# Kernel optimization log

Measured on AMD Instinct MI355X. Metric: run time of the kernel, lower is better.

Reference implementation:

```python
import jax, jax.numpy as jnp
import numpy as np

ALPHA = 1.5
N_ITER = 50
N_ROWS, N_CLASSES = 4096, 32000


def tsallis_bisect(X, alpha=ALPHA, n_iter=N_ITER):
    """Entmax/Tsallis simplex projection via 50-step bisection (matches
    the standard entmax-bisect forward used by sisl/EvSoftmax)."""
    d = X.shape[-1]
    exp = 1.0 / (alpha - 1.0)          # = 2.0 for alpha = 1.5
    Xs = X * (alpha - 1.0)
    max_val = jnp.max(Xs, axis=-1, keepdims=True)            # [N,1]
    tau_lo = max_val - 1.0
    tau_hi = max_val - (1.0 / d) ** (alpha - 1.0)
    f_lo = jnp.sum(jnp.clip(Xs - tau_lo, 0.0) ** exp, axis=-1, keepdims=True) - 1.0
    dm0 = tau_hi - tau_lo

    def body(carry, _):
        tau_lo, dm, _tau_m = carry
        dm = dm * 0.5
        tau_m = tau_lo + dm                                   # [N,1]
        p_m = jnp.clip(Xs - tau_m, 0.0) ** exp                # [N,d]
        f_m = jnp.sum(p_m, axis=-1, keepdims=True) - 1.0
        mask = (f_m * f_lo) >= 0
        tau_lo = jnp.where(mask, tau_m, tau_lo)
        return (tau_lo, dm, tau_m), None

    (_, _, tau_m), _ = jax.lax.scan(body, (tau_lo, dm0, tau_lo), None, length=n_iter)
    return jnp.clip(Xs - tau_m, 0.0) ** exp                   # final p_m


def setup_inputs() -> dict:
    key = jax.random.key(0)
    X = jax.random.normal(key, (N_ROWS, N_CLASSES), dtype=jnp.float32)
    return {"X": X}


def reference(X):
    p_star = tsallis_bisect(X, ALPHA, N_ITER)
    p_star = p_star / jnp.sum(p_star, axis=1, keepdims=True)
    # safe log: value identical to log(p_star) (log(0) = -inf), but with a
    # well-defined (zero) subgradient at exactly-sparse entries.
    return jnp.where(p_star > 0, jnp.log(jnp.where(p_star > 0, p_star, 1.0)), -jnp.inf)
```

## Files before the change

kernel.cpp:

```cpp
#include <hip/hip_runtime.h>
#include <math.h>


#define NCOLS    32000
#define TPBA     512
#define NFULL    15
#define TAILBASE 30720
#define TAILTHR  320
#define NWAVE    8
#define SEGB     320
#define CAPR     (SEGB * NWAVE)
#define NSLOT    (CAPR / 64)
#define MSEG     512
#define SENT16   ((unsigned short)0xC2C0)
#define CSF      0.0055901699437494742f

__device__ __forceinline__ float wred_max(float x) {
#pragma unroll
  for (int o = 1; o < 64; o <<= 1) x = fmaxf(x, __shfl_xor(x, o, 64));
  return x;
}
__device__ __forceinline__ float wred_addf(float x) {
#pragma unroll
  for (int o = 1; o < 64; o <<= 1) x += __shfl_xor(x, o, 64);
  return x;
}
__device__ __forceinline__ int lane_prefix(unsigned long long m) {
  return __builtin_amdgcn_mbcnt_hi((unsigned)(m >> 32),
         __builtin_amdgcn_mbcnt_lo((unsigned)m, 0));
}
__device__ __forceinline__ unsigned short to_bf16_safe(float x) {
  unsigned int u = __float_as_uint(x);
  u += 0x7FFFu + ((u >> 16) & 1u);
  unsigned short h = (unsigned short)(u >> 16);
  if ((h & 0x7F80u) == 0x7F80u) h = SENT16;
  return h;
}

__global__ __launch_bounds__(TPBA, 4)
void tsa_stream(const float* __restrict__ X, unsigned short* __restrict__ Out,
                float* __restrict__ tauv, int* __restrict__ cnt,
                float* __restrict__ vals, unsigned short* __restrict__ idxs) {
  __shared__ float s_redf[NWAVE];
  __shared__ int   s_ovf;
  const int t    = threadIdx.x;
  const int lane = t & 63;
  const int wid  = t >> 6;
  const size_t row = blockIdx.x;
  const float* __restrict__ xr      = X + row * (size_t)NCOLS;
  unsigned short* __restrict__ orow = Out + row * (size_t)NCOLS;

  float4 v[16];
#pragma unroll
  for (int j = 0; j < NFULL; ++j)
    v[j] = *reinterpret_cast<const float4*>(xr + j * 2048 + t * 4);
  if (t < TAILTHR)
    v[15] = *reinterpret_cast<const float4*>(xr + TAILBASE + t * 4);
  else
    v[15] = make_float4(-1e30f, -1e30f, -1e30f, -1e30f);
  if (t == 0) s_ovf = 0;

  float m = -1e30f;
#pragma unroll
  for (int j = 0; j < 16; ++j)
    m = fmaxf(m, fmaxf(fmaxf(v[j].x, v[j].y), fmaxf(v[j].z, v[j].w)));
  m = wred_max(m);
  if (lane == 0) s_redf[wid] = m;
  __syncthreads();
  float mm = s_redf[0];
#pragma unroll
  for (int w = 1; w < NWAVE; ++w) mm = fmaxf(mm, s_redf[w]);
  const float max_val = 0.5f * mm;
  const float tl0 = max_val - 1.0f;
  if (t == 0) tauv[row] = max_val;

  {
    int base = 0;
    float* __restrict__ vb = vals + row * (size_t)CAPR + wid * SEGB;
    unsigned short* __restrict__ ib = idxs + row * (size_t)CAPR + wid * SEGB;
#pragma unroll
    for (int j = 0; j < 16; ++j) {
      const int gidx = (j < NFULL) ? (j * 2048 + t * 4) : (TAILBASE + t * 4);
      const float xs[4] = {v[j].x * 0.5f, v[j].y * 0.5f,
                           v[j].z * 0.5f, v[j].w * 0.5f};
#pragma unroll
      for (int c = 0; c < 4; ++c) {
        const bool b = xs[c] > tl0;
        const unsigned long long mk = __ballot(b);
        const int tot = __popcll(mk);
        if (base + tot <= SEGB) {
          if (b) {
            const int pos = base + lane_prefix(mk);
            vb[pos] = xs[c];
            ib[pos] = (unsigned short)(gidx + c);
          }
        } else if (lane == 0) {
          s_ovf = 1;
        }
        base += tot;
      }
    }
    if (base <= SEGB && lane == 0) cnt[row * NWAVE + wid] = base;
  }
  __syncthreads();

  if (s_ovf) {
    if (t == 0) cnt[row * NWAVE] = -1;
    const float th = max_val - CSF;
    auto bsum = [&](float tau) -> float {
      float q = 0.f;
#pragma unroll
      for (int j = 0; j < 16; ++j) {
        float r;
        r = fmaxf(v[j].x * 0.5f - tau, 0.f); q = fmaf(r, r, q);
        r = fmaxf(v[j].y * 0.5f - tau, 0.f); q = fmaf(r, r, q);
        r = fmaxf(v[j].z * 0.5f - tau, 0.f); q = fmaf(r, r, q);
        r = fmaxf(v[j].w * 0.5f - tau, 0.f); q = fmaf(r, r, q);
      }
      q = wred_addf(q);
      if (lane == 0) s_redf[wid] = q;
      __syncthreads();
      float tt = s_redf[0];
#pragma unroll
      for (int w = 1; w < NWAVE; ++w) tt += s_redf[w];
      __syncthreads();
      return tt;
    };
    float tau_lo = tl0, dmv = th - tl0, tau_m = tl0;
    const float f_lo = bsum(tau_lo) - 1.0f;
#pragma unroll 1
    for (int it = 0; it < 50; ++it) {
      dmv *= 0.5f;
      const float tm = tau_lo + dmv;
      if (tm == tau_lo) { tau_m = tau_lo; break; }
      tau_m = tm;
      const float fm = bsum(tm) - 1.0f;
      if (fm * f_lo >= 0.0f) tau_lo = tm;
    }
    const float sf = bsum(tau_m);
#pragma unroll
    for (int j = 0; j < 16; ++j) {
      const bool act = (j < NFULL) || (t < TAILTHR);
      if (act) {
        const int gidx = (j < NFULL) ? (j * 2048 + t * 4) : (TAILBASE + t * 4);
        unsigned short h[4];
        float rc, pn;
        rc = fmaxf(v[j].x * 0.5f - tau_m, 0.f); pn = (rc * rc) / sf; h[0] = (pn > 0.f) ? to_bf16_safe(logf(pn)) : SENT16;
        rc = fmaxf(v[j].y * 0.5f - tau_m, 0.f); pn = (rc * rc) / sf; h[1] = (pn > 0.f) ? to_bf16_safe(logf(pn)) : SENT16;
        rc = fmaxf(v[j].z * 0.5f - tau_m, 0.f); pn = (rc * rc) / sf; h[2] = (pn > 0.f) ? to_bf16_safe(logf(pn)) : SENT16;
        rc = fmaxf(v[j].w * 0.5f - tau_m, 0.f); pn = (rc * rc) / sf; h[3] = (pn > 0.f) ? to_bf16_safe(logf(pn)) : SENT16;
        *reinterpret_cast<uint2*>(orow + gidx) =
            make_uint2((unsigned)h[0] | ((unsigned)h[1] << 16),
                       (unsigned)h[2] | ((unsigned)h[3] << 16));
      }
    }
  }
}

__global__ __launch_bounds__(512, 4)
void tsa_bisect(unsigned short* __restrict__ Out,
                const float* __restrict__ tauv, const int* __restrict__ cnt,
                const float* __restrict__ vals,
                const unsigned short* __restrict__ idxs, int nrows) {
  const int t    = threadIdx.x;
  const int lane = t & 63;
  const int wid  = t >> 6;
  const int row  = blockIdx.x * NWAVE + wid;
  if (row >= nrows) return;

  int c8 = (lane < NWAVE) ? cnt[row * NWAVE + lane] : 0;
  const int c0 = __shfl(c8, 0, 64);
  if (c0 < 0) return;

  unsigned short* __restrict__ orow = Out + (size_t)row * NCOLS;

  {
    const unsigned int sp = 0xC2C0C2C0u;
    const uint4 fillv = make_uint4(sp, sp, sp, sp);
    uint4* o4 = reinterpret_cast<uint4*>(orow);
#pragma unroll 1
    for (int r = 0; r < 63; ++r) {
      const int p = lane + r * 64;
      if (p < NCOLS / 8) o4[p] = fillv;
    }
  }

  const float* __restrict__ vb = vals + (size_t)row * CAPR;
  float cv[NSLOT];
#pragma unroll
  for (int r = 0; r < NSLOT; ++r) cv[r] = vb[lane + r * 64];
#pragma unroll
  for (int r = 0; r < NSLOT; ++r) {
    const int cs = __shfl(c8, r / 5, 64);
    if ((r % 5) * 64 + lane >= cs) cv[r] = -1e30f;
  }

  const float max_val = tauv[row];
  const float tl0 = max_val - 1.0f;
  const float th  = max_val - CSF;

  auto fsum = [&](float tau) -> float {
    float q0 = 0.f, q1 = 0.f, q2 = 0.f, q3 = 0.f;
#pragma unroll
    for (int r = 0; r < NSLOT; r += 4) {
      float a;
      a = fmaxf(cv[r + 0] - tau, 0.f); q0 = fmaf(a, a, q0);
      a = fmaxf(cv[r + 1] - tau, 0.f); q1 = fmaf(a, a, q1);
      a = fmaxf(cv[r + 2] - tau, 0.f); q2 = fmaf(a, a, q2);
      a = fmaxf(cv[r + 3] - tau, 0.f); q3 = fmaf(a, a, q3);
    }
    return wred_addf((q0 + q1) + (q2 + q3));
  };

  float tau_lo = tl0, dmv = th - tl0, tau_m = tl0;
  const float f_lo = fsum(tau_lo) - 1.0f;
#pragma unroll 1
  for (int it = 0; it < 50; ++it) {
    dmv *= 0.5f;
    const float tm = tau_lo + dmv;
    if (tm == tau_lo) { tau_m = tau_lo; break; }
    tau_m = tm;
    const float fm = fsum(tm) - 1.0f;
    if (fm * f_lo >= 0.0f) tau_lo = tm;
  }
  const float sf = fsum(tau_m);

  asm volatile("s_waitcnt vmcnt(0)" ::: "memory");

  const unsigned short* __restrict__ ib = idxs + (size_t)row * CAPR;
#pragma unroll 1
  for (int r = 0; r < NSLOT; ++r) {
    const float rc = fmaxf(cv[r] - tau_m, 0.f);
    const float pn = (rc * rc) / sf;
    if (pn > 0.f) orow[ib[lane + r * 64]] = to_bf16_safe(logf(pn));
  }
}

__global__ __launch_bounds__(TPBA, 8)
void tsa_mono(const float* __restrict__ X, unsigned short* __restrict__ Out) {
  __shared__ float          s_redf[NWAVE];
  __shared__ int            s_segk[NWAVE];
  __shared__ int            s_ovf;
  __shared__ float          s_tau, s_sf;
  __shared__ float          s_cand[MSEG * NWAVE];
  __shared__ unsigned short s_cidx[MSEG * NWAVE];

  const int t = threadIdx.x, lane = t & 63, wid = t >> 6;
  const size_t row = blockIdx.x;
  const float* __restrict__ xr      = X + row * (size_t)NCOLS;
  unsigned short* __restrict__ orow = Out + row * (size_t)NCOLS;

  float m = -1e30f;
#pragma unroll 5
  for (int j = 0; j < NFULL; ++j) {
    float4 a = *reinterpret_cast<const float4*>(xr + j * 2048 + t * 4);
    m = fmaxf(m, fmaxf(fmaxf(a.x, a.y), fmaxf(a.z, a.w)));
  }
  if (t < TAILTHR) {
    float4 a = *reinterpret_cast<const float4*>(xr + TAILBASE + t * 4);
    m = fmaxf(m, fmaxf(fmaxf(a.x, a.y), fmaxf(a.z, a.w)));
  }
  m = wred_max(m);
  if (lane == 0) s_redf[wid] = m;
  if (t == 0) s_ovf = 0;
  __syncthreads();
  float mm = s_redf[0];
#pragma unroll
  for (int w = 1; w < NWAVE; ++w) mm = fmaxf(mm, s_redf[w]);
  const float max_val = 0.5f * mm;
  const float tau_lo0 = max_val - 1.0f;
  const float tau_hi  = max_val - CSF;

  {
    int base = 0;
    const int seg0 = wid * MSEG;
    const unsigned long long SFILL = 0xC2C0C2C0C2C0C2C0ull;
#pragma unroll 2
    for (int j = 0; j <= NFULL; ++j) {
      const bool act = (j < NFULL) || (t < TAILTHR);
      const int gidx = (j < NFULL) ? (j * 2048 + t * 4) : (TAILBASE + t * 4);
      float x0 = -1e30f, x1 = -1e30f, x2 = -1e30f, x3 = -1e30f;
      if (act) {
        float4 a = *reinterpret_cast<const float4*>(xr + gidx);
        x0 = a.x * 0.5f; x1 = a.y * 0.5f; x2 = a.z * 0.5f; x3 = a.w * 0.5f;
        __builtin_nontemporal_store(
            SFILL, reinterpret_cast<unsigned long long*>(orow + gidx));
      }
      int c = (x0 > tau_lo0) + (x1 > tau_lo0) + (x2 > tau_lo0) + (x3 > tau_lo0);
      int pre = c;
#pragma unroll
      for (int o = 1; o < 64; o <<= 1) {
        int y = __shfl_up(pre, o, 64);
        if (lane >= o) pre += y;
      }
      const int tot = __shfl(pre, 63, 64);
      if (base + tot <= MSEG) {
        int pos = seg0 + base + (pre - c);
        if (x0 > tau_lo0) { s_cand[pos] = x0; s_cidx[pos] = (unsigned short)(gidx + 0); ++pos; }
        if (x1 > tau_lo0) { s_cand[pos] = x1; s_cidx[pos] = (unsigned short)(gidx + 1); ++pos; }
        if (x2 > tau_lo0) { s_cand[pos] = x2; s_cidx[pos] = (unsigned short)(gidx + 2); ++pos; }
        if (x3 > tau_lo0) { s_cand[pos] = x3; s_cidx[pos] = (unsigned short)(gidx + 3); ++pos; }
      } else if (lane == 0) {
        s_ovf = 1;
      }
      base += tot;
    }
    if (base <= MSEG) {
      const int kp = (base + 63) & ~63;
      for (int i = base + lane; i < kp; i += 64) s_cand[seg0 + i] = -1e30f;
    }
    if (lane == 0) s_segk[wid] = base;
  }
  __syncthreads();

  if (s_ovf == 0) {
    if (wid == 0) {
      int kp[NWAVE];
#pragma unroll
      for (int s = 0; s < NWAVE; ++s) kp[s] = (s_segk[s] + 63) & ~63;
      auto fsum = [&](float tau) -> float {
        float q = 0.f;
#pragma unroll 1
        for (int s = 0; s < NWAVE; ++s) {
          const float* cs = s_cand + s * MSEG;
          const int kps = kp[s];
          for (int i = lane; i < kps; i += 64) {
            const float r = fmaxf(cs[i] - tau, 0.f);
            q = fmaf(r, r, q);
          }
        }
        return wred_addf(q);
      };
      float tau_lo = tau_lo0, dmv = tau_hi - tau_lo0, tau_m = tau_lo0;
      const float f_lo = fsum(tau_lo) - 1.0f;
#pragma unroll 1
      for (int it = 0; it < 50; ++it) {
        dmv *= 0.5f;
        const float tm = tau_lo + dmv;
        if (tm == tau_lo) { tau_m = tau_lo; break; }
        tau_m = tm;
        const float fm = fsum(tm) - 1.0f;
        if (fm * f_lo >= 0.0f) tau_lo = tm;
      }
      const float sf = fsum(tau_m);
      if (lane == 0) { s_tau = tau_m; s_sf = sf; }
    }
    __syncthreads();
    const float tau_m = s_tau, sf = s_sf;
#pragma unroll 1
    for (int s = 0; s < NWAVE; ++s) {
      const int ks = s_segk[s];
      for (int i = t; i < ks; i += TPBA) {
        const float rc = fmaxf(s_cand[s * MSEG + i] - tau_m, 0.f);
        const float pn = (rc * rc) / sf;
        if (pn > 0.f) orow[s_cidx[s * MSEG + i]] = to_bf16_safe(logf(pn));
      }
    }
  } else {
    auto bsum = [&](float tau) -> float {
      float q = 0.f;
#pragma unroll 4
      for (int j = 0; j <= NFULL; ++j) {
        const bool act = (j < NFULL) || (t < TAILTHR);
        const int gidx = (j < NFULL) ? (j * 2048 + t * 4) : (TAILBASE + t * 4);
        if (act) {
          float4 a = *reinterpret_cast<const float4*>(xr + gidx);
          float r;
          r = fmaxf(a.x * 0.5f - tau, 0.f); q = fmaf(r, r, q);
          r = fmaxf(a.y * 0.5f - tau, 0.f); q = fmaf(r, r, q);
          r = fmaxf(a.z * 0.5f - tau, 0.f); q = fmaf(r, r, q);
          r = fmaxf(a.w * 0.5f - tau, 0.f); q = fmaf(r, r, q);
        }
      }
      q = wred_addf(q);
      if (lane == 0) s_redf[wid] = q;
      __syncthreads();
      float tot = s_redf[0];
#pragma unroll
      for (int w = 1; w < NWAVE; ++w) tot += s_redf[w];
      __syncthreads();
      return tot;
    };
    float tau_lo = tau_lo0, dmv = tau_hi - tau_lo0, tau_m = tau_lo0;
    const float f_lo = bsum(tau_lo) - 1.0f;
#pragma unroll 1
    for (int it = 0; it < 50; ++it) {
      dmv *= 0.5f;
      const float tm = tau_lo + dmv;
      if (tm == tau_lo) { tau_m = tau_lo; break; }
      tau_m = tm;
      const float fm = bsum(tm) - 1.0f;
      if (fm * f_lo >= 0.0f) tau_lo = tm;
    }
    const float sf = bsum(tau_m);
#pragma unroll 1
    for (int j = 0; j <= NFULL; ++j) {
      const bool act = (j < NFULL) || (t < TAILTHR);
      const int gidx = (j < NFULL) ? (j * 2048 + t * 4) : (TAILBASE + t * 4);
      if (act) {
        float4 a = *reinterpret_cast<const float4*>(xr + gidx);
        unsigned short h[4];
        float rc, pn;
        rc = fmaxf(a.x * 0.5f - tau_m, 0.f); pn = (rc * rc) / sf; h[0] = (pn > 0.f) ? to_bf16_safe(logf(pn)) : SENT16;
        rc = fmaxf(a.y * 0.5f - tau_m, 0.f); pn = (rc * rc) / sf; h[1] = (pn > 0.f) ? to_bf16_safe(logf(pn)) : SENT16;
        rc = fmaxf(a.z * 0.5f - tau_m, 0.f); pn = (rc * rc) / sf; h[2] = (pn > 0.f) ? to_bf16_safe(logf(pn)) : SENT16;
        rc = fmaxf(a.w * 0.5f - tau_m, 0.f); pn = (rc * rc) / sf; h[3] = (pn > 0.f) ? to_bf16_safe(logf(pn)) : SENT16;
        *reinterpret_cast<uint2*>(orow + gidx) =
            make_uint2((unsigned)h[0] | ((unsigned)h[1] << 16),
                       (unsigned)h[2] | ((unsigned)h[3] << 16));
      }
    }
  }
}

extern "C" void kernel_launch(void* const* d_in, const int* in_sizes, int n_in,
                              void* d_out, int out_size, void* d_ws, size_t ws_size,
                              hipStream_t stream) {
  const float* X = (const float*)d_in[0];
  unsigned short* Out = (unsigned short*)d_out;
  const int rows = in_sizes[0] / NCOLS;

  const size_t offT = 0;
  const size_t offC = (size_t)rows * 4;
  const size_t offV = (offC + (size_t)rows * NWAVE * 4 + 255) & ~(size_t)255;
  const size_t offI = (offV + (size_t)rows * CAPR * 4 + 255) & ~(size_t)255;
  const size_t need = offI + (size_t)rows * CAPR * 2;

  if (ws_size >= need) {
    char* ws = (char*)d_ws;
    float* tauv = (float*)(ws + offT);
    int* cnt = (int*)(ws + offC);
    float* vals = (float*)(ws + offV);
    unsigned short* idxs = (unsigned short*)(ws + offI);
    hipLaunchKernelGGL(tsa_stream, dim3(rows), dim3(TPBA), 0, stream,
                       X, Out, tauv, cnt, vals, idxs);
    const int gridB = (rows + NWAVE - 1) / NWAVE;
    hipLaunchKernelGGL(tsa_bisect, dim3(gridB), dim3(512), 0, stream,
                       Out, tauv, cnt, vals, idxs, rows);
  } else {
    hipLaunchKernelGGL(tsa_mono, dim3(rows), dim3(TPBA), 0, stream, X, Out);
  }
}
```

Measured before the change: 243.0 us.

## Assemble output rows in LDS and write them with coalesced stores

The second kernel now handles one row per block instead of one row per wave. Wave 0 runs the bisection while the other seven waves fill an LDS row buffer with the sentinel. The surviving entries are then scattered into LDS, and the finished row goes to global memory as coalesced 16-byte stores. This replaces scattered global 2-byte writes and the separate global fill, and also switches to __logf and a multiply by the reciprocal. The cost is 64KB of LDS per block, which limits occupancy, and bisection now runs on only one wave per block while the other waves sit idle after the fill.

```diff
diff --git a/kernel.cpp b/kernel.cpp
--- a/kernel.cpp
+++ b/kernel.cpp
@@ -158,81 +158,95 @@
 }
 
 __global__ __launch_bounds__(512, 4)
-void tsa_bisect(unsigned short* __restrict__ Out,
-                const float* __restrict__ tauv, const int* __restrict__ cnt,
-                const float* __restrict__ vals,
-                const unsigned short* __restrict__ idxs, int nrows) {
+void tsb_emit(unsigned short* __restrict__ Out,
+              const float* __restrict__ tauv, const int* __restrict__ cnt,
+              const float* __restrict__ vals,
+              const unsigned short* __restrict__ idxs, int nrows) {
+  __shared__ unsigned short s_row[NCOLS];
+  __shared__ int   s_cnt[NWAVE];
+  __shared__ float s_tau, s_isf;
+
   const int t    = threadIdx.x;
   const int lane = t & 63;
   const int wid  = t >> 6;
-  const int row  = blockIdx.x * NWAVE + wid;
+  const int row  = blockIdx.x;
   if (row >= nrows) return;
 
-  int c8 = (lane < NWAVE) ? cnt[row * NWAVE + lane] : 0;
-  const int c0 = __shfl(c8, 0, 64);
-  if (c0 < 0) return;
-
-  unsigned short* __restrict__ orow = Out + (size_t)row * NCOLS;
-
-  {
+  if (t < NWAVE) s_cnt[t] = cnt[row * NWAVE + t];
+  __syncthreads();
+  if (s_cnt[0] < 0) return;
+
+  if (wid == 0) {
+    int c8 = (lane < NWAVE) ? s_cnt[lane] : 0;
+    const float* __restrict__ vb = vals + (size_t)row * CAPR;
+    float cv[NSLOT];
+#pragma unroll
+    for (int r = 0; r < NSLOT; ++r) cv[r] = vb[lane + r * 64];
+#pragma unroll
+    for (int r = 0; r < NSLOT; ++r) {
+      const int cs = __shfl(c8, r / 5, 64);
+      if ((r % 5) * 64 + lane >= cs) cv[r] = -1e30f;
+    }
+    const float max_val = tauv[row];
+    const float tl0 = max_val - 1.0f;
+    const float th  = max_val - CSF;
+
+    auto fsum = [&](float tau) -> float {
+      float q0 = 0.f, q1 = 0.f, q2 = 0.f, q3 = 0.f;
+#pragma unroll
+      for (int r = 0; r < NSLOT; r += 4) {
+        float a;
+        a = fmaxf(cv[r + 0] - tau, 0.f); q0 = fmaf(a, a, q0);
+        a = fmaxf(cv[r + 1] - tau, 0.f); q1 = fmaf(a, a, q1);
+        a = fmaxf(cv[r + 2] - tau, 0.f); q2 = fmaf(a, a, q2);
+        a = fmaxf(cv[r + 3] - tau, 0.f); q3 = fmaf(a, a, q3);
+      }
+      return wred_addf((q0 + q1) + (q2 + q3));
+    };
+
+    float tau_lo = tl0, dmv = th - tl0, tau_m = tl0;
+    const float f_lo = fsum(tau_lo) - 1.0f;
+#pragma unroll 1
+    for (int it = 0; it < 50; ++it) {
+      dmv *= 0.5f;
+      const float tm = tau_lo + dmv;
+      if (tm == tau_lo) { tau_m = tau_lo; break; }
+      tau_m = tm;
+      const float fm = fsum(tm) - 1.0f;
+      if (fm * f_lo >= 0.0f) tau_lo = tm;
+    }
+    const float sf = fsum(tau_m);
+    if (lane == 0) { s_tau = tau_m; s_isf = 1.0f / sf; }
+  } else {
     const unsigned int sp = 0xC2C0C2C0u;
     const uint4 fillv = make_uint4(sp, sp, sp, sp);
-    uint4* o4 = reinterpret_cast<uint4*>(orow);
-#pragma unroll 1
-    for (int r = 0; r < 63; ++r) {
-      const int p = lane + r * 64;
-      if (p < NCOLS / 8) o4[p] = fillv;
-    }
-  }
-
+    uint4* l4 = reinterpret_cast<uint4*>(s_row);
+    for (int i = t - 64; i < NCOLS / 8; i += (512 - 64)) l4[i] = fillv;
+  }
+  __syncthreads();
+
+  const float tau_m = s_tau, isf = s_isf;
   const float* __restrict__ vb = vals + (size_t)row * CAPR;
-  float cv[NSLOT];
-#pragma unroll
-  for (int r = 0; r < NSLOT; ++r) cv[r] = vb[lane + r * 64];
-#pragma unroll
-  for (int r = 0; r < NSLOT; ++r) {
-    const int cs = __shfl(c8, r / 5, 64);
-    if ((r % 5) * 64 + lane >= cs) cv[r] = -1e30f;
-  }
-
-  const float max_val = tauv[row];
-  const float tl0 = max_val - 1.0f;
-  const float th  = max_val - CSF;
-
-  auto fsum = [&](float tau) -> float {
-    float q0 = 0.f, q1 = 0.f, q2 = 0.f, q3 = 0.f;
-#pragma unroll
-    for (int r = 0; r < NSLOT; r += 4) {
-      float a;
-      a = fmaxf(cv[r + 0] - tau, 0.f); q0 = fmaf(a, a, q0);
-      a = fmaxf(cv[r + 1] - tau, 0.f); q1 = fmaf(a, a, q1);
-      a = fmaxf(cv[r + 2] - tau, 0.f); q2 = fmaf(a, a, q2);
-      a = fmaxf(cv[r + 3] - tau, 0.f); q3 = fmaf(a, a, q3);
-    }
-    return wred_addf((q0 + q1) + (q2 + q3));
-  };
-
-  float tau_lo = tl0, dmv = th - tl0, tau_m = tl0;
-  const float f_lo = fsum(tau_lo) - 1.0f;
-#pragma unroll 1
-  for (int it = 0; it < 50; ++it) {
-    dmv *= 0.5f;
-    const float tm = tau_lo + dmv;
-    if (tm == tau_lo) { tau_m = tau_lo; break; }
-    tau_m = tm;
-    const float fm = fsum(tm) - 1.0f;
-    if (fm * f_lo >= 0.0f) tau_lo = tm;
-  }
-  const float sf = fsum(tau_m);
-
-  asm volatile("s_waitcnt vmcnt(0)" ::: "memory");
-
   const unsigned short* __restrict__ ib = idxs + (size_t)row * CAPR;
-#pragma unroll 1
-  for (int r = 0; r < NSLOT; ++r) {
-    const float rc = fmaxf(cv[r] - tau_m, 0.f);
-    const float pn = (rc * rc) / sf;
-    if (pn > 0.f) orow[ib[lane + r * 64]] = to_bf16_safe(logf(pn));
+#pragma unroll
+  for (int r = 0; r < CAPR / 512; ++r) {
+    const int slot = t + r * 512;
+    const int seg = slot / SEGB, off = slot % SEGB;
+    if (off < s_cnt[seg]) {
+      const float rc = fmaxf(vb[slot] - tau_m, 0.f);
+      const float pn = rc * rc * isf;
+      if (pn > 0.f) s_row[ib[slot]] = to_bf16_safe(__logf(pn));
+    }
+  }
+  __syncthreads();
+
+  unsigned short* __restrict__ orow = Out + (size_t)row * NCOLS;
+  uint4* og = reinterpret_cast<uint4*>(orow);
+  const uint4* l4 = reinterpret_cast<const uint4*>(s_row);
+#pragma unroll
+  for (int r = 0; r < 8; ++r) {
+    const int i = t + r * 512;
+    if (i < NCOLS / 8) og[i] = l4[i];
   }
 }
 
@@ -434,8 +448,7 @@
     unsigned short* idxs = (unsigned short*)(ws + offI);
     hipLaunchKernelGGL(tsa_stream, dim3(rows), dim3(TPBA), 0, stream,
                        X, Out, tauv, cnt, vals, idxs);
-    const int gridB = (rows + NWAVE - 1) / NWAVE;
-    hipLaunchKernelGGL(tsa_bisect, dim3(gridB), dim3(512), 0, stream,
+    hipLaunchKernelGGL(tsb_emit, dim3(rows), dim3(512), 0, stream,
                        Out, tauv, cnt, vals, idxs, rows);
   } else {
     hipLaunchKernelGGL(tsa_mono, dim3(rows), dim3(TPBA), 0, stream, X, Out);
```

New measurement: 282.9 us. 16.4% more time.

## Move sentinel fill into streaming kernel and coalesce sparse output writes

Applied to the files above, without the earlier changes.

The full-row sentinel fill moves out of the per-row bisection kernel and into the streaming kernel as nontemporal stores, issued right after the row is loaded. The bisection kernel then writes each 32-element chunk that holds candidates as four 16-byte stores, instead of scattering single 2-byte stores into a pre-filled row. Candidate compaction switches to per-lane ballot and popcount ranks, which keeps each segment in ascending column order so chunk grouping works. The prefix scan in the monolithic kernel is replaced the same way. The code also uses a reciprocal and fast __logf, and adds serial per-chunk loops with long branch chains in exchange.

```diff
diff --git a/kernel.cpp b/kernel.cpp
--- a/kernel.cpp
+++ b/kernel.cpp
@@ -25,10 +25,6 @@
   for (int o = 1; o < 64; o <<= 1) x += __shfl_xor(x, o, 64);
   return x;
 }
-__device__ __forceinline__ int lane_prefix(unsigned long long m) {
-  return __builtin_amdgcn_mbcnt_hi((unsigned)(m >> 32),
-         __builtin_amdgcn_mbcnt_lo((unsigned)m, 0));
-}
 __device__ __forceinline__ unsigned short to_bf16_safe(float x) {
   unsigned int u = __float_as_uint(x);
   u += 0x7FFFu + ((u >> 16) & 1u);
@@ -58,6 +54,16 @@
     v[15] = *reinterpret_cast<const float4*>(xr + TAILBASE + t * 4);
   else
     v[15] = make_float4(-1e30f, -1e30f, -1e30f, -1e30f);
+
+  {
+    const unsigned long long SF = 0xC2C0C2C0C2C0C2C0ull;
+    unsigned long long* o8 = reinterpret_cast<unsigned long long*>(orow);
+#pragma unroll
+    for (int i = 0; i < 16; ++i) {
+      const int p = t + i * TPBA;
+      if (p < NCOLS / 4) __builtin_nontemporal_store(SF, o8 + p);
+    }
+  }
   if (t == 0) s_ovf = 0;
 
   float m = -1e30f;
@@ -78,27 +84,27 @@
     int base = 0;
     float* __restrict__ vb = vals + row * (size_t)CAPR + wid * SEGB;
     unsigned short* __restrict__ ib = idxs + row * (size_t)CAPR + wid * SEGB;
+    const unsigned long long lm = (1ull << lane) - 1ull;
 #pragma unroll
     for (int j = 0; j < 16; ++j) {
       const int gidx = (j < NFULL) ? (j * 2048 + t * 4) : (TAILBASE + t * 4);
-      const float xs[4] = {v[j].x * 0.5f, v[j].y * 0.5f,
-                           v[j].z * 0.5f, v[j].w * 0.5f};
-#pragma unroll
-      for (int c = 0; c < 4; ++c) {
-        const bool b = xs[c] > tl0;
-        const unsigned long long mk = __ballot(b);
-        const int tot = __popcll(mk);
-        if (base + tot <= SEGB) {
-          if (b) {
-            const int pos = base + lane_prefix(mk);
-            vb[pos] = xs[c];
-            ib[pos] = (unsigned short)(gidx + c);
-          }
-        } else if (lane == 0) {
-          s_ovf = 1;
-        }
-        base += tot;
-      }
+      const float x0 = v[j].x * 0.5f, x1 = v[j].y * 0.5f;
+      const float x2 = v[j].z * 0.5f, x3 = v[j].w * 0.5f;
+      const bool f0 = x0 > tl0, f1 = x1 > tl0, f2 = x2 > tl0, f3 = x3 > tl0;
+      const unsigned long long m0 = __ballot(f0), m1 = __ballot(f1);
+      const unsigned long long m2 = __ballot(f2), m3 = __ballot(f3);
+      const int tot = __popcll(m0) + __popcll(m1) + __popcll(m2) + __popcll(m3);
+      if (base + tot <= SEGB) {
+        int pos = base + __popcll(m0 & lm) + __popcll(m1 & lm) +
+                         __popcll(m2 & lm) + __popcll(m3 & lm);
+        if (f0) { vb[pos] = x0; ib[pos] = (unsigned short)(gidx + 0); ++pos; }
+        if (f1) { vb[pos] = x1; ib[pos] = (unsigned short)(gidx + 1); ++pos; }
+        if (f2) { vb[pos] = x2; ib[pos] = (unsigned short)(gidx + 2); ++pos; }
+        if (f3) { vb[pos] = x3; ib[pos] = (unsigned short)(gidx + 3); ++pos; }
+      } else if (lane == 0) {
+        s_ovf = 1;
+      }
+      base += tot;
     }
     if (base <= SEGB && lane == 0) cnt[row * NWAVE + wid] = base;
   }
@@ -172,20 +178,8 @@
   const int c0 = __shfl(c8, 0, 64);
   if (c0 < 0) return;
 
-  unsigned short* __restrict__ orow = Out + (size_t)row * NCOLS;
-
-  {
-    const unsigned int sp = 0xC2C0C2C0u;
-    const uint4 fillv = make_uint4(sp, sp, sp, sp);
-    uint4* o4 = reinterpret_cast<uint4*>(orow);
-#pragma unroll 1
-    for (int r = 0; r < 63; ++r) {
-      const int p = lane + r * 64;
-      if (p < NCOLS / 8) o4[p] = fillv;
-    }
-  }
-
   const float* __restrict__ vb = vals + (size_t)row * CAPR;
+
   float cv[NSLOT];
 #pragma unroll
   for (int r = 0; r < NSLOT; ++r) cv[r] = vb[lane + r * 64];
@@ -224,15 +218,54 @@
     if (fm * f_lo >= 0.0f) tau_lo = tm;
   }
   const float sf = fsum(tau_m);
-
-  asm volatile("s_waitcnt vmcnt(0)" ::: "memory");
-
+  const float isf = 1.0f / sf;
+
+  unsigned short* __restrict__ orow = Out + (size_t)row * NCOLS;
   const unsigned short* __restrict__ ib = idxs + (size_t)row * CAPR;
-#pragma unroll 1
-  for (int r = 0; r < NSLOT; ++r) {
-    const float rc = fmaxf(cv[r] - tau_m, 0.f);
-    const float pn = (rc * rc) / sf;
-    if (pn > 0.f) orow[ib[lane + r * 64]] = to_bf16_safe(logf(pn));
+  const unsigned sp = 0xC2C0C2C0u;
+
+#pragma unroll 1
+  for (int s = 0; s < NWAVE; ++s) {
+    const int cs = __shfl(c8, s, 64);
+    const int sb = s * SEGB;
+#pragma unroll 1
+    for (int off = lane; off < cs; off += 64) {
+      const int L = ((int)ib[sb + off]) >> 5;
+      if (off > 0 && (((int)ib[sb + off - 1]) >> 5) == L) continue;
+      uint4 w0 = make_uint4(sp, sp, sp, sp), w1 = w0, w2 = w0, w3 = w0;
+#pragma unroll 1
+      for (int q = off; q < cs; ++q) {
+        const int iq = (int)ib[sb + q];
+        if ((iq >> 5) != L) break;
+        const float rc = fmaxf(vb[sb + q] - tau_m, 0.f);
+        const float pn = rc * rc * isf;
+        if (pn > 0.f) {
+          const unsigned short hh = to_bf16_safe(__logf(pn));
+          const int pos = iq & 31;
+          const int wi  = pos >> 1;
+          const unsigned hv = (pos & 1) ? ((unsigned)hh << 16) : (unsigned)hh;
+          const unsigned km = (pos & 1) ? 0x0000FFFFu : 0xFFFF0000u;
+          if      (wi ==  0) w0.x = (w0.x & km) | hv;
+          else if (wi ==  1) w0.y = (w0.y & km) | hv;
+          else if (wi ==  2) w0.z = (w0.z & km) | hv;
+          else if (wi ==  3) w0.w = (w0.w & km) | hv;
+          else if (wi ==  4) w1.x = (w1.x & km) | hv;
+          else if (wi ==  5) w1.y = (w1.y & km) | hv;
+          else if (wi ==  6) w1.z = (w1.z & km) | hv;
+          else if (wi ==  7) w1.w = (w1.w & km) | hv;
+          else if (wi ==  8) w2.x = (w2.x & km) | hv;
+          else if (wi ==  9) w2.y = (w2.y & km) | hv;
+          else if (wi == 10) w2.z = (w2.z & km) | hv;
+          else if (wi == 11) w2.w = (w2.w & km) | hv;
+          else if (wi == 12) w3.x = (w3.x & km) | hv;
+          else if (wi == 13) w3.y = (w3.y & km) | hv;
+          else if (wi == 14) w3.z = (w3.z & km) | hv;
+          else               w3.w = (w3.w & km) | hv;
+        }
+      }
+      uint4* dst = reinterpret_cast<uint4*>(orow + (L << 5));
+      dst[0] = w0; dst[1] = w1; dst[2] = w2; dst[3] = w3;
+    }
   }
 }
 
@@ -275,6 +308,7 @@
     int base = 0;
     const int seg0 = wid * MSEG;
     const unsigned long long SFILL = 0xC2C0C2C0C2C0C2C0ull;
+    const unsigned long long lm = (1ull << lane) - 1ull;
 #pragma unroll 2
     for (int j = 0; j <= NFULL; ++j) {
       const bool act = (j < NFULL) || (t < TAILTHR);
@@ -286,20 +320,18 @@
         __builtin_nontemporal_store(
             SFILL, reinterpret_cast<unsigned long long*>(orow + gidx));
       }
-      int c = (x0 > tau_lo0) + (x1 > tau_lo0) + (x2 > tau_lo0) + (x3 > tau_lo0);
-      int pre = c;
-#pragma unroll
-      for (int o = 1; o < 64; o <<= 1) {
-        int y = __shfl_up(pre, o, 64);
-        if (lane >= o) pre += y;
-      }
-      const int tot = __shfl(pre, 63, 64);
+      const bool f0 = x0 > tau_lo0, f1 = x1 > tau_lo0;
+      const bool f2 = x2 > tau_lo0, f3 = x3 > tau_lo0;
+      const unsigned long long m0 = __ballot(f0), m1 = __ballot(f1);
+      const unsigned long long m2 = __ballot(f2), m3 = __ballot(f3);
+      const int tot = __popcll(m0) + __popcll(m1) + __popcll(m2) + __popcll(m3);
       if (base + tot <= MSEG) {
-        int pos = seg0 + base + (pre - c);
-        if (x0 > tau_lo0) { s_cand[pos] = x0; s_cidx[pos] = (unsigned short)(gidx + 0); ++pos; }
-        if (x1 > tau_lo0) { s_cand[pos] = x1; s_cidx[pos] = (unsigned short)(gidx + 1); ++pos; }
-        if (x2 > tau_lo0) { s_cand[pos] = x2; s_cidx[pos] = (unsigned short)(gidx + 2); ++pos; }
-        if (x3 > tau_lo0) { s_cand[pos] = x3; s_cidx[pos] = (unsigned short)(gidx + 3); ++pos; }
+        int pos = seg0 + base + __popcll(m0 & lm) + __popcll(m1 & lm) +
+                                __popcll(m2 & lm) + __popcll(m3 & lm);
+        if (f0) { s_cand[pos] = x0; s_cidx[pos] = (unsigned short)(gidx + 0); ++pos; }
+        if (f1) { s_cand[pos] = x1; s_cidx[pos] = (unsigned short)(gidx + 1); ++pos; }
+        if (f2) { s_cand[pos] = x2; s_cidx[pos] = (unsigned short)(gidx + 2); ++pos; }
+        if (f3) { s_cand[pos] = x3; s_cidx[pos] = (unsigned short)(gidx + 3); ++pos; }
       } else if (lane == 0) {
         s_ovf = 1;
       }
```

After: 302.1 us. 24.3% more time.
